# Kernel optimization log

Hardware: AMD Instinct MI355X
Metric: run time of the kernel (lower is better)

## Reference

```python
import jax, jax.numpy as jnp
import numpy as np

EMBED_DIM = 512
NUM_HEADS = 8
HEAD_DIM = EMBED_DIM // NUM_HEADS


def setup_inputs() -> dict:
    key = jax.random.key(0)
    k_x, k_qkv, k_proj, k_pb = jax.random.split(key, 4)
    B, N, C = 2, 4096, EMBED_DIM
    x = jax.random.normal(k_x, (B, N, C), dtype=jnp.float32)
    # nn.Linear(embed_dim, 3*embed_dim, bias=False): weight [3C, C], y = x @ W.T
    s = 1.0 / np.sqrt(C)
    w_qkv = jax.random.uniform(k_qkv, (3 * C, C), dtype=jnp.float32, minval=-s, maxval=s)
    w_proj = jax.random.uniform(k_proj, (C, C), dtype=jnp.float32, minval=-s, maxval=s)
    b_proj = jax.random.uniform(k_pb, (C,), dtype=jnp.float32, minval=-s, maxval=s)
    return {"x": x, "w_qkv": w_qkv, "w_proj": w_proj, "b_proj": b_proj}


def reference(x, w_qkv, w_proj, b_proj):
    B, N, C = x.shape
    H, D = NUM_HEADS, HEAD_DIM
    scale = D ** -0.5
    qkv = jnp.einsum('bnc,fc->bnf', x, w_qkv)           # [B, N, 3C]
    qkv = qkv.reshape(B, N, 3, H, D)
    q, k, v = [jnp.transpose(qkv[:, :, i], (0, 2, 1, 3)) for i in range(3)]  # [B,H,N,D]
    attn = jnp.einsum('bhnd,bhmd->bhnm', q, k) * scale  # [B,H,N,N]
    # additive causal mask: -inf above the diagonal
    causal = jnp.triu(jnp.full((N, N), -jnp.inf, dtype=attn.dtype), k=1)
    attn = jax.nn.softmax(attn + causal, axis=-1)
    out = jnp.einsum('bhnm,bhmd->bhnd', attn, v)        # [B,H,N,D]
    out = jnp.transpose(out, (0, 2, 1, 3)).reshape(B, N, C)
    return jnp.einsum('bnc,oc->bno', out, w_proj) + b_proj
```

## Files before the change

### kernel.cpp

```cpp
#include <hip/hip_runtime.h>
#include <hip/hip_bf16.h>


typedef __attribute__((ext_vector_type(8))) short s16x8;
typedef __attribute__((ext_vector_type(4))) float f32x4;
typedef __attribute__((ext_vector_type(16))) float f32x16;
typedef __attribute__((ext_vector_type(4))) unsigned u32x4;

#define QSCALE 0.18033688011112042f

__device__ __forceinline__ ushort f2bf(float f) {
  unsigned u = __float_as_uint(f);
  u = (u + 0x7FFFu + ((u >> 16) & 1u)) >> 16;
  return (ushort)u;
}

__device__ __forceinline__ unsigned cvt_pk_bf16(float a, float b) {
  unsigned r;
  asm("v_cvt_pk_bf16_f32 %0, %1, %2" : "=v"(r) : "v"(a), "v"(b));
  return r;
}

__device__ __forceinline__ float bflo(unsigned u) { return __uint_as_float(u << 16); }
__device__ __forceinline__ float bfhi(unsigned u) { return __uint_as_float(u & 0xffff0000u); }

__global__ __launch_bounds__(256) void cvt_all(const float* __restrict__ x,
                                               const float* __restrict__ wq,
                                               const float* __restrict__ wp,
                                               ushort* __restrict__ xb,
                                               ushort* __restrict__ wqb,
                                               ushort* __restrict__ wpb) {
  int i = blockIdx.x * 256 + threadIdx.x;
  const float* src;
  ushort* dst;
  int off;
  if (i < 1048576) {
    src = x; dst = xb; off = i;
  } else if (i < 1245184) {
    src = wq; dst = wqb; off = i - 1048576;
  } else {
    src = wp; dst = wpb; off = i - 1245184;
  }
  float4 v = reinterpret_cast<const float4*>(src)[off];
  ushort4 o;
  o.x = f2bf(v.x); o.y = f2bf(v.y); o.z = f2bf(v.z); o.w = f2bf(v.w);
  reinterpret_cast<ushort4*>(dst)[off] = o;
}

template <int EPI>
__global__ __launch_bounds__(256) void gemm_bt(const ushort* __restrict__ A,
                                               const ushort* __restrict__ W,
                                               ushort* __restrict__ q_ws,
                                               ushort* __restrict__ k_ws,
                                               ushort* __restrict__ vt_ws,
                                               float* __restrict__ outf,
                                               const float* __restrict__ bias) {
  __shared__ ushort As[2][128 * 32];
  __shared__ ushort Bs[2][128 * 32];
  const int tid = threadIdx.x;
  const int lane = tid & 63, wv = tid >> 6;
  const int wm = wv >> 1, wn = wv & 1;
  const int l15 = lane & 15, g = lane >> 4;
  const int tm = blockIdx.y * 128, tn = blockIdx.x * 128;

  f32x4 acc[4][4] = {};

#define GSTAGE(BUF, K0)                                                                    \
  do {                                                                                     \
    _Pragma("unroll") for (int it = 0; it < 2; ++it) {                                     \
      int slot = it * 256 + tid;                                                           \
      int row = slot >> 2;                                                                 \
      int ch = (slot & 3) ^ ((row >> 1) & 3);                                              \
      const int sb = (it * 256 + wv * 64) * 8;        \
      __builtin_amdgcn_global_load_lds(                                                    \
          (const __attribute__((address_space(1))) void*)(A + (size_t)(tm + row) * 512 +   \
                                                          (K0) + ch * 8),                  \
          (__attribute__((address_space(3))) void*)(&As[BUF][0] + sb), 16, 0, 0);          \
      __builtin_amdgcn_global_load_lds(                                                    \
          (const __attribute__((address_space(1))) void*)(W + (size_t)(tn + row) * 512 +   \
                                                          (K0) + ch * 8),                  \
          (__attribute__((address_space(3))) void*)(&Bs[BUF][0] + sb), 16, 0, 0);          \
    }                                                                                      \
  } while (0)

  GSTAGE(0, 0);
  __syncthreads();
  int cur = 0;
  for (int t = 0; t < 16; ++t) {
    if (t < 15) GSTAGE(cur ^ 1, (t + 1) * 32);
    s16x8 af[4], bfr[4];
#pragma unroll
    for (int i = 0; i < 4; ++i) {
      int Ra = wm * 64 + i * 16 + l15;
      af[i] = reinterpret_cast<const s16x8*>(&As[cur][0])[Ra * 4 + (g ^ ((Ra >> 1) & 3))];
      int Rb = wn * 64 + i * 16 + l15;
      bfr[i] = reinterpret_cast<const s16x8*>(&Bs[cur][0])[Rb * 4 + (g ^ ((Rb >> 1) & 3))];
    }
#pragma unroll
    for (int mi = 0; mi < 4; ++mi)
#pragma unroll
      for (int ni = 0; ni < 4; ++ni)
        acc[mi][ni] =
            __builtin_amdgcn_mfma_f32_16x16x32_bf16(af[mi], bfr[ni], acc[mi][ni], 0, 0, 0);
    __syncthreads();
    cur ^= 1;
  }
#undef GSTAGE

  const int rowb = tm + wm * 64 + g * 4;
  const int colb = tn + wn * 64 + l15;
#pragma unroll
  for (int mi = 0; mi < 4; ++mi) {
#pragma unroll
    for (int ni = 0; ni < 4; ++ni) {
      int r0 = rowb + mi * 16;
      int col = colb + ni * 16;
      if (EPI == 0) {
        int i3 = col >> 9, h = (col >> 6) & 7, d = col & 63;
        int b = r0 >> 12;
        int bh = b * 8 + h;
        if (i3 == 2) {
          int n0 = r0 & 4095;
          int kt64 = n0 >> 6, key64 = n0 & 63;
          int kc = key64 >> 4, hk = (key64 >> 3) & 1, j0 = key64 & 7;
          int db = d >> 5, d31 = d & 31;
          ushort4 pk;
          pk.x = f2bf(acc[mi][ni][0]);
          pk.y = f2bf(acc[mi][ni][1]);
          pk.z = f2bf(acc[mi][ni][2]);
          pk.w = f2bf(acc[mi][ni][3]);
          *reinterpret_cast<ushort4*>(vt_ws + (size_t)(bh * 64 + kt64) * 4096 +
                                      ((db * 4 + kc) * 64 + d31 + 32 * hk) * 8 + j0) = pk;
        } else if (i3 == 1) {
          int dt = d >> 4, hd = (d >> 3) & 1, j = d & 7;
#pragma unroll
          for (int r = 0; r < 4; ++r) {
            int n = (r0 + r) & 4095;
            int kt64 = n >> 6, key64 = n & 63;
            int kb = key64 >> 5, key31 = key64 & 31;
            k_ws[(size_t)(bh * 64 + kt64) * 4096 +
                 ((kb * 4 + dt) * 64 + key31 + 32 * hd) * 8 + j] = f2bf(acc[mi][ni][r]);
          }
        } else {
          int dt = d >> 4, hd = (d >> 3) & 1, j = d & 7;
#pragma unroll
          for (int r = 0; r < 4; ++r) {
            int n = (r0 + r) & 4095;
            int qt = n >> 5, q31 = n & 31;
            q_ws[(size_t)(bh * 128 + qt) * 2048 + (dt * 64 + q31 + 32 * hd) * 8 + j] =
                f2bf(acc[mi][ni][r] * QSCALE);
          }
        }
      } else {
#pragma unroll
        for (int r = 0; r < 4; ++r)
          outf[(size_t)(r0 + r) * 512 + col] = acc[mi][ni][r] + bias[col];
      }
    }
  }
}

__global__ __launch_bounds__(256, 4) void attn_kernel(const ushort* __restrict__ Q,
                                                      const ushort* __restrict__ Kk,
                                                      const ushort* __restrict__ Vt,
                                                      ushort* __restrict__ po,
                                                      float* __restrict__ ml) {
  __shared__ ushort Ks[2][4096];
  __shared__ ushort Vs[2][4096];
  const int tid = threadIdx.x;
  const int lane = tid & 63, wv = tid >> 6;
  const int l31 = lane & 31, hf = lane >> 5;
  const int L = blockIdx.x;
  const int p = L & 7;
  int j2 = L >> 3;
  {
    const int pos = j2 & 31, quarter = j2 >> 5;
    if (quarter & 1) j2 = quarter * 32 + (31 - pos);
  }
  const int bh = p * 2 + (j2 & 1);
  const int i = j2 >> 1;
  const int G = 31 - (i >> 1);
  const int h = i & 1;
  const int qt = 4 * G + wv;
  const int ktmax = qt >> 1;
  const int mid = G + 1;
  const int klo = h ? mid : 0;
  const int khi = h ? ktmax : (mid - 1);
  const int KLO = h ? mid : 0;
  const int KHI = h ? (2 * G + 1) : (mid - 1);
  const int slot = (bh * 128 + qt) * 2 + h;
  const int qw = qt * 32;

  s16x8 aq[4];
  {
    const ushort* qp = Q + ((size_t)bh * 128 + qt) * 2048 + lane * 8;
#pragma unroll
    for (int dt = 0; dt < 4; ++dt) aq[dt] = *reinterpret_cast<const s16x8*>(qp + dt * 512);
  }

  f32x16 o[2] = {};
  float m = -1e30f;
  float l = 0.f;

#define KVSTAGE(BUF, KT)                                                                  \
  do {                                                                                    \
    const ushort* kSrc = Kk + ((size_t)bh * 64 + (KT)) * 4096;                            \
    const ushort* vSrc = Vt + ((size_t)bh * 64 + (KT)) * 4096;                            \
    _Pragma("unroll") for (int c = 0; c < 2; ++c) {                                       \
      const int sb = (c * 256 + wv * 64) * 8;                                             \
      __builtin_amdgcn_global_load_lds(                                                   \
          (const __attribute__((address_space(1))) void*)(kSrc + sb + lane * 8),          \
          (__attribute__((address_space(3))) void*)(&Ks[BUF][0] + sb), 16, 0, 0);         \
      __builtin_amdgcn_global_load_lds(                                                   \
          (const __attribute__((address_space(1))) void*)(vSrc + sb + lane * 8),          \
          (__attribute__((address_space(3))) void*)(&Vs[BUF][0] + sb), 16, 0, 0);         \
    }                                                                                     \
  } while (0)

  KVSTAGE(0, KLO);
  __syncthreads();
  int cur = 0;
  for (int kt = KLO; kt <= KHI; ++kt) {
    if (kt < KHI) KVSTAGE(cur ^ 1, kt + 1);
    if (kt >= klo && kt <= khi) {
      const ushort* kl = &Ks[cur][lane * 8];
      s16x8 kf[8];
#pragma unroll
      for (int t = 0; t < 8; ++t) kf[t] = *reinterpret_cast<const s16x8*>(kl + t * 512);
      f32x16 st[2] = {};
      __builtin_amdgcn_s_setprio(1);
#pragma unroll
      for (int kb = 0; kb < 2; ++kb)
#pragma unroll
        for (int dt = 0; dt < 4; ++dt)
          st[kb] = __builtin_amdgcn_mfma_f32_32x32x16_bf16(kf[kb * 4 + dt], aq[dt],
                                                           st[kb], 0, 0, 0);
      __builtin_amdgcn_s_setprio(0);
      if (kt == ktmax) {
        const int qg = qw + l31;
#pragma unroll
        for (int kb = 0; kb < 2; ++kb)
#pragma unroll
          for (int r = 0; r < 16; ++r)
            if (kt * 64 + kb * 32 + (r & 3) + 8 * (r >> 2) + 4 * hf > qg)
              st[kb][r] = -1e30f;
      }
      float mx[2];
#pragma unroll
      for (int kb = 0; kb < 2; ++kb) {
        float t0 = fmaxf(fmaxf(st[kb][0], st[kb][1]), fmaxf(st[kb][2], st[kb][3]));
        float t1 = fmaxf(fmaxf(st[kb][4], st[kb][5]), fmaxf(st[kb][6], st[kb][7]));
        float t2 = fmaxf(fmaxf(st[kb][8], st[kb][9]), fmaxf(st[kb][10], st[kb][11]));
        float t3 = fmaxf(fmaxf(st[kb][12], st[kb][13]), fmaxf(st[kb][14], st[kb][15]));
        mx[kb] = fmaxf(fmaxf(t0, t1), fmaxf(t2, t3));
      }
      float pm = fmaxf(mx[0], mx[1]);
      if (!__all(pm - m <= 8.0f)) {
        float pmf = fmaxf(pm, __shfl_xor(pm, 32));
        const float mn = fmaxf(m, pmf);
        const float al = __builtin_amdgcn_exp2f(m - mn);
        l *= al;
        m = mn;
#pragma unroll
        for (int db = 0; db < 2; ++db)
#pragma unroll
          for (int r = 0; r < 16; ++r) o[db][r] *= al;
      }
      s16x8 pb[4];
      float rs = 0.f;
#pragma unroll
      for (int kb = 0; kb < 2; ++kb) {
        float e[16];
#pragma unroll
        for (int r = 0; r < 16; ++r) {
          e[r] = __builtin_amdgcn_exp2f(st[kb][r] - m);
          rs += e[r];
        }
        unsigned a0 = cvt_pk_bf16(e[0], e[1]), a1 = cvt_pk_bf16(e[2], e[3]);
        unsigned b0 = cvt_pk_bf16(e[4], e[5]), b1 = cvt_pk_bf16(e[6], e[7]);
        asm volatile("v_permlane32_swap_b32 %0, %1" : "+v"(a0), "+v"(b0));
        asm volatile("v_permlane32_swap_b32 %0, %1" : "+v"(a1), "+v"(b1));
        u32x4 w0;
        w0[0] = a0; w0[1] = a1; w0[2] = b0; w0[3] = b1;
        pb[kb * 2] = __builtin_bit_cast(s16x8, w0);
        unsigned c0 = cvt_pk_bf16(e[8], e[9]), c1 = cvt_pk_bf16(e[10], e[11]);
        unsigned d0 = cvt_pk_bf16(e[12], e[13]), d1 = cvt_pk_bf16(e[14], e[15]);
        asm volatile("v_permlane32_swap_b32 %0, %1" : "+v"(c0), "+v"(d0));
        asm volatile("v_permlane32_swap_b32 %0, %1" : "+v"(c1), "+v"(d1));
        u32x4 w1;
        w1[0] = c0; w1[1] = c1; w1[2] = d0; w1[3] = d1;
        pb[kb * 2 + 1] = __builtin_bit_cast(s16x8, w1);
      }
      l += rs;
      const ushort* vl = &Vs[cur][lane * 8];
      s16x8 vf[8];
#pragma unroll
      for (int t = 0; t < 8; ++t) vf[t] = *reinterpret_cast<const s16x8*>(vl + t * 512);
      __builtin_amdgcn_s_setprio(1);
#pragma unroll
      for (int db = 0; db < 2; ++db)
#pragma unroll
        for (int kc = 0; kc < 4; ++kc)
          o[db] = __builtin_amdgcn_mfma_f32_32x32x16_bf16(vf[db * 4 + kc], pb[kc],
                                                          o[db], 0, 0, 0);
      __builtin_amdgcn_s_setprio(0);
    }
    __syncthreads();
    cur ^= 1;
  }
#undef KVSTAGE

  float lr = l + __shfl_xor(l, 32);
  const float linv = (lr > 0.f) ? (1.0f / lr) : 0.f;

  const size_t pbase = ((size_t)slot * 32 + l31) * 64;
#pragma unroll
  for (int db = 0; db < 2; ++db)
#pragma unroll
    for (int rg = 0; rg < 4; ++rg) {
      const int d0 = db * 32 + 8 * rg + 4 * hf;
      uint2 pk;
      pk.x = cvt_pk_bf16(o[db][rg * 4 + 0] * linv, o[db][rg * 4 + 1] * linv);
      pk.y = cvt_pk_bf16(o[db][rg * 4 + 2] * linv, o[db][rg * 4 + 3] * linv);
      *reinterpret_cast<uint2*>(po + pbase + d0) = pk;
    }
  if (hf == 0) {
    float2 v;
    v.x = m;
    v.y = lr;
    *reinterpret_cast<float2*>(ml + ((size_t)slot * 32 + l31) * 2) = v;
  }
}

__global__ __launch_bounds__(64) void attn_merge(const ushort* __restrict__ po,
                                                 const float* __restrict__ ml,
                                                 ushort* __restrict__ O) {
  const int M = blockIdx.x, tid = threadIdx.x;
  const int p = M & 7, q2 = M >> 3;
  const int bh = p * 2 + (q2 & 1);
  const int qt = q2 >> 1;
  const int t = bh * 128 + qt;
  const int row = tid >> 1, dh = (tid & 1) * 32;
  const float2 ml0 = *reinterpret_cast<const float2*>(ml + ((size_t)(t * 2 + 0) * 32 + row) * 2);
  const float2 ml1 = *reinterpret_cast<const float2*>(ml + ((size_t)(t * 2 + 1) * 32 + row) * 2);
  const float ms = fmaxf(ml0.x, ml1.x);
  const float w0 = __builtin_amdgcn_exp2f(ml0.x - ms) * ml0.y;
  const float w1 = __builtin_amdgcn_exp2f(ml1.x - ms) * ml1.y;
  const float inv = 1.0f / (w0 + w1);
  const float c0 = w0 * inv, c1 = w1 * inv;
  const int b = bh >> 3, h = bh & 7;
  const size_t rowo = (size_t)(b * 4096 + qt * 32 + row) * 512 + h * 64 + dh;
  const ushort* p0 = po + ((size_t)(t * 2 + 0) * 32 + row) * 64 + dh;
  const ushort* p1 = po + ((size_t)(t * 2 + 1) * 32 + row) * 64 + dh;
#pragma unroll
  for (int j = 0; j < 4; ++j) {
    uint4 a = reinterpret_cast<const uint4*>(p0)[j];
    uint4 bb = reinterpret_cast<const uint4*>(p1)[j];
    uint4 out;
    out.x = cvt_pk_bf16(c0 * bflo(a.x) + c1 * bflo(bb.x), c0 * bfhi(a.x) + c1 * bfhi(bb.x));
    out.y = cvt_pk_bf16(c0 * bflo(a.y) + c1 * bflo(bb.y), c0 * bfhi(a.y) + c1 * bfhi(bb.y));
    out.z = cvt_pk_bf16(c0 * bflo(a.z) + c1 * bflo(bb.z), c0 * bfhi(a.z) + c1 * bfhi(bb.z));
    out.w = cvt_pk_bf16(c0 * bflo(a.w) + c1 * bflo(bb.w), c0 * bfhi(a.w) + c1 * bfhi(bb.w));
    reinterpret_cast<uint4*>(&O[rowo])[j] = out;
  }
}

extern "C" void kernel_launch(void* const* d_in, const int* in_sizes, int n_in,
                              void* d_out, int out_size, void* d_ws, size_t ws_size,
                              hipStream_t stream) {
  const float* x = (const float*)d_in[0];
  const float* w_qkv = (const float*)d_in[1];
  const float* w_proj = (const float*)d_in[2];
  const float* b_proj = (const float*)d_in[3];
  float* out = (float*)d_out;

  ushort* xb = (ushort*)d_ws;
  ushort* wqkvb = xb + (size_t)8192 * 512;
  ushort* wprojb = wqkvb + (size_t)1536 * 512;
  ushort* qws = wprojb + (size_t)512 * 512;
  ushort* kws = qws + (size_t)16 * 4096 * 64;
  ushort* vtws = kws + (size_t)16 * 4096 * 64;
  ushort* ows = vtws + (size_t)16 * 4096 * 64;

  cvt_all<<<5120, 256, 0, stream>>>(x, w_qkv, w_proj, xb, wqkvb, wprojb);

  gemm_bt<0><<<dim3(12, 64), 256, 0, stream>>>(xb, wqkvb, qws, kws, vtws, nullptr, nullptr);

  ushort* po = ows + (size_t)8192 * 512;
  float* ml = (float*)(po + (size_t)2048 * 2 * 32 * 64);

  attn_kernel<<<1024, 256, 0, stream>>>(qws, kws, vtws, po, ml);
  attn_merge<<<2048, 64, 0, stream>>>(po, ml, ows);

  gemm_bt<1><<<dim3(4, 64), 256, 0, stream>>>(ows, wprojb, nullptr, nullptr, nullptr, out,
                                              b_proj);
}
```

Baseline: 103.9 us.

## Split causal attention KV range into variable chunks per query group

Replaces the fixed two-way KV split with a variable split, where later query groups get up to four KV chunks. The grid grows from 1024 to 1280 blocks, with the longest-work blocks scheduled first, to balance load across CUs. The merge kernel now combines up to four partial results using their max and sum statistics, and the launch bound is raised to 5 blocks per CU. The cost is extra partial-output traffic, more merge work, and possible register pressure from the occupancy hint.

```diff
diff --git a/kernel.cpp b/kernel.cpp
--- a/kernel.cpp
+++ b/kernel.cpp
@@ -160,7 +160,7 @@
   }
 }
 
-__global__ __launch_bounds__(256, 4) void attn_kernel(const ushort* __restrict__ Q,
+__global__ __launch_bounds__(256, 5) void attn_kernel(const ushort* __restrict__ Q,
                                                       const ushort* __restrict__ Kk,
                                                       const ushort* __restrict__ Vt,
                                                       ushort* __restrict__ po,
@@ -172,23 +172,23 @@
   const int l31 = lane & 31, hf = lane >> 5;
   const int L = blockIdx.x;
   const int p = L & 7;
-  int j2 = L >> 3;
-  {
-    const int pos = j2 & 31, quarter = j2 >> 5;
-    if (quarter & 1) j2 = quarter * 32 + (31 - pos);
-  }
+  const int j2 = L >> 3;
   const int bh = p * 2 + (j2 & 1);
-  const int i = j2 >> 1;
-  const int G = 31 - (i >> 1);
-  const int h = i & 1;
+  const int idx = 79 - (j2 >> 1);
+  int G = 31, s = idx;
+  for (int g = 0; g < 32; ++g) {
+    int Sg = (g >> 3) + 1;
+    if (s < Sg) { G = g; break; }
+    s -= Sg;
+  }
+  const int S = (G >> 3) + 1;
+  const int T = 2 * G + 2;
+  const int klo = s * T / S;
+  const int khi = (s + 1) * T / S - 1;
   const int qt = 4 * G + wv;
   const int ktmax = qt >> 1;
-  const int mid = G + 1;
-  const int klo = h ? mid : 0;
-  const int khi = h ? ktmax : (mid - 1);
-  const int KLO = h ? mid : 0;
-  const int KHI = h ? (2 * G + 1) : (mid - 1);
-  const int slot = (bh * 128 + qt) * 2 + h;
+  const int khi_w = (khi < ktmax) ? khi : ktmax;
+  const int slot = bh * 80 + idx;
   const int qw = qt * 32;
 
   s16x8 aq[4];
@@ -217,12 +217,12 @@
     }                                                                                     \
   } while (0)
 
-  KVSTAGE(0, KLO);
+  KVSTAGE(0, klo);
   __syncthreads();
   int cur = 0;
-  for (int kt = KLO; kt <= KHI; ++kt) {
-    if (kt < KHI) KVSTAGE(cur ^ 1, kt + 1);
-    if (kt >= klo && kt <= khi) {
+  for (int kt = klo; kt <= khi; ++kt) {
+    if (kt < khi) KVSTAGE(cur ^ 1, kt + 1);
+    if (kt <= khi_w) {
       const ushort* kl = &Ks[cur][lane * 8];
       s16x8 kf[8];
 #pragma unroll
@@ -313,7 +313,7 @@
   float lr = l + __shfl_xor(l, 32);
   const float linv = (lr > 0.f) ? (1.0f / lr) : 0.f;
 
-  const size_t pbase = ((size_t)slot * 32 + l31) * 64;
+  const size_t pbase = ((size_t)slot * 128 + wv * 32 + l31) * 64;
 #pragma unroll
   for (int db = 0; db < 2; ++db)
 #pragma unroll
@@ -328,7 +328,7 @@
     float2 v;
     v.x = m;
     v.y = lr;
-    *reinterpret_cast<float2*>(ml + ((size_t)slot * 32 + l31) * 2) = v;
+    *reinterpret_cast<float2*>(ml + ((size_t)slot * 128 + wv * 32 + l31) * 2) = v;
   }
 }
 
@@ -339,28 +339,67 @@
   const int p = M & 7, q2 = M >> 3;
   const int bh = p * 2 + (q2 & 1);
   const int qt = q2 >> 1;
-  const int t = bh * 128 + qt;
-  const int row = tid >> 1, dh = (tid & 1) * 32;
-  const float2 ml0 = *reinterpret_cast<const float2*>(ml + ((size_t)(t * 2 + 0) * 32 + row) * 2);
-  const float2 ml1 = *reinterpret_cast<const float2*>(ml + ((size_t)(t * 2 + 1) * 32 + row) * 2);
-  const float ms = fmaxf(ml0.x, ml1.x);
-  const float w0 = __builtin_amdgcn_exp2f(ml0.x - ms) * ml0.y;
-  const float w1 = __builtin_amdgcn_exp2f(ml1.x - ms) * ml1.y;
-  const float inv = 1.0f / (w0 + w1);
-  const float c0 = w0 * inv, c1 = w1 * inv;
+  const int G = qt >> 2;
+  const int a = G >> 3, bq = G & 7;
+  const int S = a + 1;
+  const int slotBase = bh * 80 + (G + 4 * a * (a - 1) + a * bq);
+  const int rowOff = (qt & 3) * 32 + (tid >> 1);
+  const int dh = (tid & 1) * 32;
+  float2 v0 = *reinterpret_cast<const float2*>(ml + ((size_t)(slotBase + 0) * 128 + rowOff) * 2);
+  float2 v1 = {-1e30f, 0.f}, v2 = {-1e30f, 0.f}, v3 = {-1e30f, 0.f};
+  if (S > 1) v1 = *reinterpret_cast<const float2*>(ml + ((size_t)(slotBase + 1) * 128 + rowOff) * 2);
+  if (S > 2) v2 = *reinterpret_cast<const float2*>(ml + ((size_t)(slotBase + 2) * 128 + rowOff) * 2);
+  if (S > 3) v3 = *reinterpret_cast<const float2*>(ml + ((size_t)(slotBase + 3) * 128 + rowOff) * 2);
+  const float ms = fmaxf(fmaxf(v0.x, v1.x), fmaxf(v2.x, v3.x));
+  float c0 = __builtin_amdgcn_exp2f(v0.x - ms) * v0.y;
+  float c1 = __builtin_amdgcn_exp2f(v1.x - ms) * v1.y;
+  float c2 = __builtin_amdgcn_exp2f(v2.x - ms) * v2.y;
+  float c3 = __builtin_amdgcn_exp2f(v3.x - ms) * v3.y;
+  const float inv = 1.0f / ((c0 + c1) + (c2 + c3));
+  c0 *= inv; c1 *= inv; c2 *= inv; c3 *= inv;
   const int b = bh >> 3, h = bh & 7;
-  const size_t rowo = (size_t)(b * 4096 + qt * 32 + row) * 512 + h * 64 + dh;
-  const ushort* p0 = po + ((size_t)(t * 2 + 0) * 32 + row) * 64 + dh;
-  const ushort* p1 = po + ((size_t)(t * 2 + 1) * 32 + row) * 64 + dh;
+  const size_t rowo = (size_t)(b * 4096 + qt * 32 + (tid >> 1)) * 512 + h * 64 + dh;
+  const ushort* p0 = po + ((size_t)(slotBase + 0) * 128 + rowOff) * 64 + dh;
+  const ushort* p1 = po + ((size_t)(slotBase + 1) * 128 + rowOff) * 64 + dh;
+  const ushort* p2 = po + ((size_t)(slotBase + 2) * 128 + rowOff) * 64 + dh;
+  const ushort* p3 = po + ((size_t)(slotBase + 3) * 128 + rowOff) * 64 + dh;
 #pragma unroll
   for (int j = 0; j < 4; ++j) {
-    uint4 a = reinterpret_cast<const uint4*>(p0)[j];
-    uint4 bb = reinterpret_cast<const uint4*>(p1)[j];
+    float acc0 = 0.f, acc1 = 0.f, acc2 = 0.f, acc3 = 0.f;
+    float acc4 = 0.f, acc5 = 0.f, acc6 = 0.f, acc7 = 0.f;
+    {
+      uint4 aa = reinterpret_cast<const uint4*>(p0)[j];
+      acc0 += c0 * bflo(aa.x); acc1 += c0 * bfhi(aa.x);
+      acc2 += c0 * bflo(aa.y); acc3 += c0 * bfhi(aa.y);
+      acc4 += c0 * bflo(aa.z); acc5 += c0 * bfhi(aa.z);
+      acc6 += c0 * bflo(aa.w); acc7 += c0 * bfhi(aa.w);
+    }
+    if (S > 1) {
+      uint4 aa = reinterpret_cast<const uint4*>(p1)[j];
+      acc0 += c1 * bflo(aa.x); acc1 += c1 * bfhi(aa.x);
+      acc2 += c1 * bflo(aa.y); acc3 += c1 * bfhi(aa.y);
+      acc4 += c1 * bflo(aa.z); acc5 += c1 * bfhi(aa.z);
+      acc6 += c1 * bflo(aa.w); acc7 += c1 * bfhi(aa.w);
+    }
+    if (S > 2) {
+      uint4 aa = reinterpret_cast<const uint4*>(p2)[j];
+      acc0 += c2 * bflo(aa.x); acc1 += c2 * bfhi(aa.x);
+      acc2 += c2 * bflo(aa.y); acc3 += c2 * bfhi(aa.y);
+      acc4 += c2 * bflo(aa.z); acc5 += c2 * bfhi(aa.z);
+      acc6 += c2 * bflo(aa.w); acc7 += c2 * bfhi(aa.w);
+    }
+    if (S > 3) {
+      uint4 aa = reinterpret_cast<const uint4*>(p3)[j];
+      acc0 += c3 * bflo(aa.x); acc1 += c3 * bfhi(aa.x);
+      acc2 += c3 * bflo(aa.y); acc3 += c3 * bfhi(aa.y);
+      acc4 += c3 * bflo(aa.z); acc5 += c3 * bfhi(aa.z);
+      acc6 += c3 * bflo(aa.w); acc7 += c3 * bfhi(aa.w);
+    }
     uint4 out;
-    out.x = cvt_pk_bf16(c0 * bflo(a.x) + c1 * bflo(bb.x), c0 * bfhi(a.x) + c1 * bfhi(bb.x));
-    out.y = cvt_pk_bf16(c0 * bflo(a.y) + c1 * bflo(bb.y), c0 * bfhi(a.y) + c1 * bfhi(bb.y));
-    out.z = cvt_pk_bf16(c0 * bflo(a.z) + c1 * bflo(bb.z), c0 * bfhi(a.z) + c1 * bfhi(bb.z));
-    out.w = cvt_pk_bf16(c0 * bflo(a.w) + c1 * bflo(bb.w), c0 * bfhi(a.w) + c1 * bfhi(bb.w));
+    out.x = cvt_pk_bf16(acc0, acc1);
+    out.y = cvt_pk_bf16(acc2, acc3);
+    out.z = cvt_pk_bf16(acc4, acc5);
+    out.w = cvt_pk_bf16(acc6, acc7);
     reinterpret_cast<uint4*>(&O[rowo])[j] = out;
   }
 }
@@ -387,9 +426,9 @@
   gemm_bt<0><<<dim3(12, 64), 256, 0, stream>>>(xb, wqkvb, qws, kws, vtws, nullptr, nullptr);
 
   ushort* po = ows + (size_t)8192 * 512;
-  float* ml = (float*)(po + (size_t)2048 * 2 * 32 * 64);
-
-  attn_kernel<<<1024, 256, 0, stream>>>(qws, kws, vtws, po, ml);
+  float* ml = (float*)(po + (size_t)1280 * 128 * 64);
+
+  attn_kernel<<<1280, 256, 0, stream>>>(qws, kws, vtws, po, ml);
   attn_merge<<<2048, 64, 0, stream>>>(po, ml, ows);
 
   gemm_bt<1><<<dim3(4, 64), 256, 0, stream>>>(ows, wprojb, nullptr, nullptr, nullptr, out,
```

Measured after the change: 366.5 us. 253% more time.
